# Performance work log

Measured on AMD Instinct MI355X. Metric: run time of the kernel, lower is better.

## Reference

```python
import jax, jax.numpy as jnp
import numpy as np

NUM_HEADS = 8
NUM_KV_HEADS = 1
HEAD_DIM = 256
ROPE_THETA = 10000.0


def setup_inputs() -> dict:
    key = jax.random.key(0)
    ks = jax.random.split(key, 5)
    B, S, H = 4, 2048, 2048
    hidden_states = jax.random.normal(ks[0], (B, S, H), dtype=jnp.float32)
    # Linear weights stored as (in_features, out_features); y = x @ W
    scale = 0.02
    Wq = jax.random.normal(ks[1], (H, NUM_HEADS * HEAD_DIM), dtype=jnp.float32) * scale
    Wk = jax.random.normal(ks[2], (H, NUM_KV_HEADS * HEAD_DIM), dtype=jnp.float32) * scale
    Wv = jax.random.normal(ks[3], (H, NUM_KV_HEADS * HEAD_DIM), dtype=jnp.float32) * scale
    Wo = jax.random.normal(ks[4], (NUM_HEADS * HEAD_DIM, H), dtype=jnp.float32) * scale
    position_ids = jnp.broadcast_to(jnp.arange(S, dtype=jnp.int64), (B, S))
    return {"hidden_states": hidden_states, "Wq": Wq, "Wk": Wk, "Wv": Wv,
            "Wo": Wo, "position_ids": position_ids}


def _rotate_half(x):
    h = x.shape[-1] // 2
    return jnp.concatenate([-x[..., h:], x[..., :h]], axis=-1)


def _rope_cos_sin(position_ids, head_dim, theta):
    # inv_freq: [head_dim/2]
    inv_freq = 1.0 / (theta ** (jnp.arange(0, head_dim, 2, dtype=jnp.float32) / head_dim))
    freqs = position_ids.astype(jnp.float32)[..., None] * inv_freq  # [B,S,hd/2]
    emb = jnp.concatenate([freqs, freqs], axis=-1)                   # [B,S,hd]
    # shape [B,1,S,hd] to broadcast over heads
    return jnp.cos(emb)[:, None], jnp.sin(emb)[:, None]


def reference(hidden_states, Wq, Wk, Wv, Wo, position_ids):
    B, S, H = hidden_states.shape
    groups = NUM_HEADS // NUM_KV_HEADS

    q = (hidden_states @ Wq).reshape(B, S, NUM_HEADS, HEAD_DIM).transpose(0, 2, 1, 3)
    k = (hidden_states @ Wk).reshape(B, S, NUM_KV_HEADS, HEAD_DIM).transpose(0, 2, 1, 3)
    v = (hidden_states @ Wv).reshape(B, S, NUM_KV_HEADS, HEAD_DIM).transpose(0, 2, 1, 3)

    cos, sin = _rope_cos_sin(position_ids, HEAD_DIM, ROPE_THETA)
    q = q * cos + _rotate_half(q) * sin
    k = k * cos + _rotate_half(k) * sin

    # GQA: repeat kv heads to match query heads
    k = jnp.repeat(k, groups, axis=1)  # [B,Hq,S,hd]
    v = jnp.repeat(v, groups, axis=1)

    scores = jnp.einsum('bhqd,bhkd->bhqk', q, k) / jnp.sqrt(jnp.float32(HEAD_DIM))
    causal = position_ids[:, None, :, None] >= position_ids[:, None, None, :]  # [B,1,S,S]
    scores = jnp.where(causal, scores, jnp.float32(-1e9))
    attn = jax.nn.softmax(scores, axis=-1)

    out = jnp.einsum('bhqk,bhkd->bhqd', attn, v)             # [B,H,S,hd]
    out = out.transpose(0, 2, 1, 3).reshape(B, S, NUM_HEADS * HEAD_DIM)
    return out @ Wo
```

## Files before the change

kernel.cpp:

```cpp
#include <hip/hip_runtime.h>
#include <hip/hip_bf16.h>

typedef __bf16 bf16;
typedef __bf16 bf16x8 __attribute__((ext_vector_type(8)));
typedef __bf16 bf16x4 __attribute__((ext_vector_type(4)));
typedef float f32x4 __attribute__((ext_vector_type(4)));

#define NB 4
#define SEQ 2048
#define HID 2048
#define NHEAD 8
#define HDIM 256
#define MTOT (NB*SEQ)

#define WAIT_VM8()  asm volatile("s_waitcnt vmcnt(8)" ::: "memory")
#define WAIT_VM0()  asm volatile("s_waitcnt vmcnt(0)" ::: "memory")

__device__ __forceinline__ void gl_lds16(const void* g, void* l) {
  __builtin_amdgcn_global_load_lds(
      (const __attribute__((address_space(1))) void*)g,
      (__attribute__((address_space(3))) void*)l, 16, 0, 0);
}

__global__ __launch_bounds__(256)
void prologue_kernel(const float* __restrict__ hs, bf16* __restrict__ Xb,
                     const float* __restrict__ Wq, bf16* __restrict__ WqT,
                     const float* __restrict__ Wo, bf16* __restrict__ WoT,
                     const float* __restrict__ Wk, bf16* __restrict__ WkT,
                     const float* __restrict__ Wv, bf16* __restrict__ WvT,
                     float2* __restrict__ tab)
{
  __shared__ float tile[32][33];
  const int bid = blockIdx.x;
  const int t = threadIdx.x;

  if (bid < 8192) {
    size_t i = (size_t)(bid * 256 + t) * 8;
    float4 v0 = *(const float4*)(hs + i);
    float4 v1 = *(const float4*)(hs + i + 4);
    bf16x8 o;
    o[0]=(bf16)v0.x; o[1]=(bf16)v0.y; o[2]=(bf16)v0.z; o[3]=(bf16)v0.w;
    o[4]=(bf16)v1.x; o[5]=(bf16)v1.y; o[6]=(bf16)v1.z; o[7]=(bf16)v1.w;
    *(bf16x8*)(Xb + i) = o;
  } else if (bid < 17408) {
    const float* in; bf16* out; int R, C, bx, by;
    if (bid < 16384) {
      int id = bid - 8192;
      int z = id >> 12, r = id & 4095;
      in = z ? Wo : Wq; out = z ? WoT : WqT; R = 2048; C = 2048;
      bx = (r & 63) * 32; by = (r >> 6) * 32;
    } else {
      int id = bid - 16384;
      int z = id >> 9, r = id & 511;
      in = z ? Wv : Wk; out = z ? WvT : WkT; R = 2048; C = 256;
      bx = (r & 7) * 32; by = (r >> 3) * 32;
    }
    int tx = t & 31, ty = t >> 5;
    #pragma unroll
    for (int k = 0; k < 4; k++)
      tile[ty + 8*k][tx] = in[(size_t)(by + ty + 8*k) * C + bx + tx];
    __syncthreads();
    #pragma unroll
    for (int k = 0; k < 4; k++)
      out[(size_t)(bx + ty + 8*k) * R + by + tx] = (bf16)tile[tx][ty + 8*k];
  } else {
    int i = (bid - 17408) * 256 + t;
    int s = i >> 7, p = i & 127;
    float invf = powf(10000.0f, -(float)p * (1.0f / 128.0f));
    float ang = (float)s * invf;
    float sn, cs;
    sincosf(ang, &sn, &cs);
    tab[i] = make_float2(cs, sn);
  }
}

template<int EPI>
__global__ __launch_bounds__(512, 2)
void gemm256_kernel(const bf16* __restrict__ A, const bf16* __restrict__ Bt,
                    void* __restrict__ Cout, int N, int K,
                    const float2* __restrict__ tab,
                    const bf16* __restrict__ Bt2,
                    bf16* __restrict__ Kout, bf16* __restrict__ VTout)
{
  __shared__ bf16 Albs[2][256 * 64];
  __shared__ bf16 Blbs[2][256 * 64];
  const int t = threadIdx.x, lane = t & 63, w = t >> 6;
  const int g = lane >> 4, c = lane & 15;
  const int wm = w >> 2, wn = w & 3;
  const int bx = blockIdx.x;
  const int m0 = blockIdx.y * 256;

  const bf16* Ab = A + (size_t)m0 * K;
  const bf16* Bb;
  int n0;
  if (EPI == 4 && bx >= 8) { Bb = Bt2 + (size_t)(bx - 8) * 256 * K; n0 = (bx - 8) * 256; }
  else                     { Bb = Bt  + (size_t)bx * 256 * K;       n0 = bx * 256; }

  auto stage = [&](const bf16* G, int k0, bf16* lds) {
    #pragma unroll
    for (int it = 0; it < 4; ++it) {
      int slot = it * 512 + t;
      int row = slot >> 3, part = (slot & 7) ^ (row & 7);
      gl_lds16(G + (size_t)row * K + k0 + part * 8, lds + (it * 512 + w * 64) * 8);
    }
  };

  f32x4 acc[8][4];
  #pragma unroll
  for (int i = 0; i < 8; i++)
    #pragma unroll
    for (int j = 0; j < 4; j++)
      acc[i][j] = (f32x4){0.f, 0.f, 0.f, 0.f};

  stage(Ab, 0, &Albs[0][0]);
  stage(Bb, 0, &Blbs[0][0]);
  __builtin_amdgcn_sched_barrier(0);

  const int NT = K >> 6;
  #pragma unroll 1
  for (int kt = 0; kt < NT; ++kt) {
    const int buf = kt & 1;
    if (kt + 1 < NT) {
      stage(Ab, (kt + 1) * 64, &Albs[buf ^ 1][0]);
      stage(Bb, (kt + 1) * 64, &Blbs[buf ^ 1][0]);
    }
    __builtin_amdgcn_sched_barrier(0);
    if (kt + 1 < NT) { WAIT_VM8(); } else { WAIT_VM0(); }
    __builtin_amdgcn_s_barrier();
    __builtin_amdgcn_sched_barrier(0);

    #pragma unroll
    for (int s2 = 0; s2 < 2; s2++) {
      bf16x8 bfr[4];
      #pragma unroll
      for (int j = 0; j < 4; j++) {
        int row = (EPI == 3 || EPI == 4) ? (wn * 16 + (j & 1) * 64 + (j >> 1) * 128 + c)
                                         : (wn * 64 + j * 16 + c);
        bfr[j] = *(const bf16x8*)((const char*)&Blbs[buf][0] + row * 128 +
                                  ((s2 * 64 + g * 16) ^ ((c & 7) * 16)));
      }
      #pragma unroll
      for (int i = 0; i < 8; i++) {
        int row = wm * 128 + i * 16 + c;
        const bf16x8 af = *(const bf16x8*)((const char*)&Albs[buf][0] + row * 128 +
                                           ((s2 * 64 + g * 16) ^ ((c & 7) * 16)));
        #pragma unroll
        for (int j = 0; j < 4; j++)
          acc[i][j] = __builtin_amdgcn_mfma_f32_16x16x32_bf16(af, bfr[j], acc[i][j], 0, 0, 0);
      }
    }
    __builtin_amdgcn_s_barrier();
  }

  if constexpr (EPI == 4) {
    if (bx < 8) {
      #pragma unroll
      for (int i = 0; i < 8; i++) {
        #pragma unroll
        for (int rr = 0; rr < 4; rr++) {
          int m = m0 + wm * 128 + i * 16 + g * 4 + rr;
          int s = m & (SEQ - 1);
          bf16* orow = (bf16*)Cout + (size_t)m * N + n0;
          #pragma unroll
          for (int jp = 0; jp < 2; jp++) {
            int d = wn * 16 + jp * 64 + c;
            float2 cs = tab[s * 128 + d];
            float vlo = acc[i][jp][rr], vhi = acc[i][jp | 2][rr];
            orow[d]       = (bf16)(vlo * cs.x - vhi * cs.y);
            orow[d + 128] = (bf16)(vhi * cs.x + vlo * cs.y);
          }
        }
      }
    } else if (bx == 8) {
      #pragma unroll
      for (int i = 0; i < 8; i++) {
        #pragma unroll
        for (int rr = 0; rr < 4; rr++) {
          int m = m0 + wm * 128 + i * 16 + g * 4 + rr;
          int s = m & (SEQ - 1);
          bf16* orow = Kout + (size_t)m * 256;
          #pragma unroll
          for (int jp = 0; jp < 2; jp++) {
            int d = wn * 16 + jp * 64 + c;
            float2 cs = tab[s * 128 + d];
            float vlo = acc[i][jp][rr], vhi = acc[i][jp | 2][rr];
            orow[d]       = (bf16)(vlo * cs.x - vhi * cs.y);
            orow[d + 128] = (bf16)(vhi * cs.x + vlo * cs.y);
          }
        }
      }
    } else {
      #pragma unroll
      for (int i = 0; i < 8; i++) {
        #pragma unroll
        for (int rr = 0; rr < 4; rr++) {
          int m = m0 + wm * 128 + i * 16 + g * 4 + rr;
          int b = m >> 11, s = m & 2047;
          #pragma unroll
          for (int j = 0; j < 4; j++) {
            int cl = wn * 16 + (j & 1) * 64 + (j >> 1) * 128 + c;
            VTout[((size_t)b * 256 + cl) * SEQ + s] = (bf16)acc[i][j][rr];
          }
        }
      }
    }
  } else {
    #pragma unroll
    for (int i = 0; i < 8; i++) {
      #pragma unroll
      for (int j = 0; j < 4; j++) {
        #pragma unroll
        for (int rr = 0; rr < 4; rr++) {
          int m = m0 + wm * 128 + i * 16 + g * 4 + rr;
          int col = n0 + wn * 64 + j * 16 + c;
          float v = acc[i][j][rr];
          if constexpr (EPI == 0) ((bf16*)Cout)[(size_t)m * N + col] = (bf16)v;
          else                    ((float*)Cout)[(size_t)m * N + col] = v;
        }
      }
    }
  }
}

__global__ __launch_bounds__(512, 2)
void attn_kernel(const bf16* __restrict__ Q, const bf16* __restrict__ Kb,
                 const bf16* __restrict__ VT, bf16* __restrict__ O)
{
  __shared__ bf16 Klds[2][64 * 256];
  __shared__ bf16 Vlds[2][256 * 64];
  __shared__ bf16 Plds[8][16 * 64];

  const int L = blockIdx.x + ((int)gridDim.x) * blockIdx.y;
  const int xcd = L & 7, slot = L >> 3;
  const int b = xcd >> 1;
  const int rem = ((xcd & 1) << 5) | slot;
  const int h = rem >> 3;
  const int p = rem & 7;

  const int t = threadIdx.x, lane = t & 63, w = t >> 6;
  const int g = lane >> 4, c = lane & 15;

  const bf16* Kbase = Kb + (size_t)b * SEQ * HDIM;
  const bf16* Vbase = VT + (size_t)b * HDIM * SEQ;

  bf16x8 ones8;
  #pragma unroll
  for (int z = 0; z < 8; z++) ones8[z] = (bf16)1.0f;

  auto stageK = [&](int kt, int buf) {
    const int kv0 = kt * 64;
    #pragma unroll
    for (int it = 0; it < 4; ++it) {
      int slot2 = it * 512 + t;
      int krow = slot2 >> 5, kpart = (slot2 & 31) ^ (krow & 7);
      gl_lds16(Kbase + (size_t)(kv0 + krow) * HDIM + kpart * 8,
               &Klds[buf][0] + (it * 512 + w * 64) * 8);
    }
  };
  auto stageV = [&](int kt, int buf) {
    const int kv0 = kt * 64;
    #pragma unroll
    for (int it = 0; it < 4; ++it) {
      int slot2 = it * 512 + t;
      int vrow = slot2 >> 3, vpart = (slot2 & 7) ^ (vrow & 7);
      gl_lds16(Vbase + (size_t)vrow * SEQ + kv0 + vpart * 8,
               &Vlds[buf][0] + (it * 512 + w * 64) * 8);
    }
  };

  #pragma unroll 1
  for (int pass = 0; pass < 2; ++pass) {
    const int qt = pass ? (15 - p) : p;
    const int q0 = qt * 128;
    const int last = 2 * qt + 1;

    bf16x8 qf[8];
    const bf16* qp = Q + (size_t)(b * SEQ + q0 + w * 16 + c) * (NHEAD * HDIM) + h * HDIM + g * 8;
    #pragma unroll
    for (int s = 0; s < 8; s++) qf[s] = *(const bf16x8*)(qp + s * 32);
    __builtin_amdgcn_sched_barrier(0);

    stageK(0, 0);
    stageV(0, 0);
    __builtin_amdgcn_sched_barrier(0);

    f32x4 acc[16];
    #pragma unroll
    for (int f = 0; f < 16; f++) acc[f] = (f32x4){0.f, 0.f, 0.f, 0.f};
    f32x4 acc_s = (f32x4){0.f, 0.f, 0.f, 0.f};

    #pragma unroll 1
    for (int kt = 0; kt <= last; ++kt) {
      const int kv0 = kt * 64;
      const int buf = kt & 1;

      if (kt < last) { stageK(kt + 1, buf ^ 1); stageV(kt + 1, buf ^ 1); }
      __builtin_amdgcn_sched_barrier(0);
      if (kt < last) { WAIT_VM8(); } else { WAIT_VM0(); }
      __builtin_amdgcn_s_barrier();
      __builtin_amdgcn_sched_barrier(0);

      const int qrow_min = q0 + w * 16;
      if (kv0 <= qrow_min + 15) {
        f32x4 sc[4];
        #pragma unroll
        for (int j = 0; j < 4; j++) sc[j] = (f32x4){0.f, 0.f, 0.f, 0.f};
        __builtin_amdgcn_s_setprio(1);
        #pragma unroll
        for (int s = 0; s < 8; s++) {
          #pragma unroll
          for (int j = 0; j < 4; j++) {
            const bf16x8 kf = *(const bf16x8*)((const char*)&Klds[buf][0] + (j * 16 + c) * 512 +
                                               ((s * 64 + g * 16) ^ ((c & 7) * 16)));
            sc[j] = __builtin_amdgcn_mfma_f32_16x16x32_bf16(qf[s], kf, sc[j], 0, 0, 0);
          }
        }
        __builtin_amdgcn_s_setprio(0);

        const float C1 = 0.09016844f;
        const float C2 = 11.54156036f;
        const bool diag = (kv0 + 63 > qrow_min);
        #pragma unroll
        for (int rr = 0; rr < 4; rr++) {
          const int row = g * 4 + rr;
          const int qrow = qrow_min + row;
          #pragma unroll
          for (int j = 0; j < 4; j++) {
            float e = exp2f(__builtin_fmaf(sc[j][rr], C1, -C2));
            if (diag && (kv0 + j * 16 + c > qrow)) e = 0.f;
            *(bf16*)((char*)&Plds[w][0] + row * 128 + (((j * 32) + c * 2) ^ ((row & 7) << 4))) = (bf16)e;
          }
        }

        #pragma unroll
        for (int s2 = 0; s2 < 2; s2++) {
          const bf16x8 pf = *(const bf16x8*)((const char*)&Plds[w][0] + c * 128 +
                                             (((s2 * 4 + g) << 4) ^ ((c & 7) << 4)));
          __builtin_amdgcn_s_setprio(1);
          #pragma unroll
          for (int f = 0; f < 16; f++) {
            const bf16x8 vf = *(const bf16x8*)((const char*)&Vlds[buf][0] + (f * 16 + c) * 128 +
                                               ((s2 * 64 + g * 16) ^ ((c & 7) * 16)));
            acc[f] = __builtin_amdgcn_mfma_f32_16x16x32_bf16(pf, vf, acc[f], 0, 0, 0);
          }
          acc_s = __builtin_amdgcn_mfma_f32_16x16x32_bf16(pf, ones8, acc_s, 0, 0, 0);
          __builtin_amdgcn_s_setprio(0);
        }
      }

      __builtin_amdgcn_s_barrier();
    }

    #pragma unroll
    for (int rr = 0; rr < 4; rr++) {
      float inv = 1.0f / acc_s[rr];
      #pragma unroll
      for (int f = 0; f < 16; f++) {
        float v = acc[f][rr] * inv;
        O[(size_t)(b * SEQ + q0 + w * 16 + g * 4 + rr) * (NHEAD * HDIM) + h * HDIM + f * 16 + c] = (bf16)v;
      }
    }
  }
}

extern "C" void kernel_launch(void* const* d_in, const int* in_sizes, int n_in,
                              void* d_out, int out_size, void* d_ws, size_t ws_size,
                              hipStream_t stream) {
  const float* hs = (const float*)d_in[0];
  const float* Wq = (const float*)d_in[1];
  const float* Wk = (const float*)d_in[2];
  const float* Wv = (const float*)d_in[3];
  const float* Wo = (const float*)d_in[4];

  char* ws = (char*)d_ws;
  bf16* Xb   = (bf16*)(ws + 0);
  bf16* WqT  = (bf16*)(ws + 33554432);
  bf16* WkT  = (bf16*)(ws + 41943040);
  bf16* WvT  = (bf16*)(ws + 42991616);
  bf16* WoT  = (bf16*)(ws + 44040192);
  bf16* Qb   = (bf16*)(ws + 52428800);
  bf16* Kb   = (bf16*)(ws + 85983232);
  bf16* VTb  = (bf16*)(ws + 90177536);
  float2* tab = (float2*)(ws + 94371840);

  prologue_kernel<<<18432, 256, 0, stream>>>(hs, Xb, Wq, WqT, Wo, WoT,
                                             Wk, WkT, Wv, WvT, tab);

  gemm256_kernel<4><<<dim3(10, 32), 512, 0, stream>>>(Xb, WqT, (void*)Qb, 2048, 2048,
                                                      tab, WkT, Kb, VTb);

  attn_kernel<<<dim3(8, 32), 512, 0, stream>>>(Qb, Kb, VTb, Xb );

  gemm256_kernel<2><<<dim3(8, 32), 512, 0, stream>>>(Xb, WoT, d_out, 2048, 2048,
                                                     nullptr, nullptr, nullptr, nullptr);
}
```

Before: 354.9 us.

## Fold K/V projection into Q GEMM blocks as a second small-tile pass

The QKV projection grid shrinks from 10x32 to 8x32 blocks. After its Q tile, each block runs a second GEMM pass over a 64-row by 256-column slice of the K or V projection, with its own RoPE or transposed-V epilogue. The goal is to remove the 64 extra K/V blocks, which overflowed one wave of 256 blocks and formed a tail wave. In exchange every block does a second, less efficient small-tile loop with a shorter A stage and a vmcnt(5) wait.

```diff
diff --git a/kernel.cpp b/kernel.cpp
--- a/kernel.cpp
+++ b/kernel.cpp
@@ -14,6 +14,7 @@
 #define MTOT (NB*SEQ)
 
 #define WAIT_VM8()  asm volatile("s_waitcnt vmcnt(8)" ::: "memory")
+#define WAIT_VM5()  asm volatile("s_waitcnt vmcnt(5)" ::: "memory")
 #define WAIT_VM0()  asm volatile("s_waitcnt vmcnt(0)" ::: "memory")
 
 __device__ __forceinline__ void gl_lds16(const void* g, void* l) {
@@ -88,13 +89,10 @@
   const int g = lane >> 4, c = lane & 15;
   const int wm = w >> 2, wn = w & 3;
   const int bx = blockIdx.x;
-  const int m0 = blockIdx.y * 256;
+  const int m0 = blockIdx.y * 256, n0 = bx * 256;
 
   const bf16* Ab = A + (size_t)m0 * K;
-  const bf16* Bb;
-  int n0;
-  if (EPI == 4 && bx >= 8) { Bb = Bt2 + (size_t)(bx - 8) * 256 * K; n0 = (bx - 8) * 256; }
-  else                     { Bb = Bt  + (size_t)bx * 256 * K;       n0 = bx * 256; }
+  const bf16* Bb = Bt + (size_t)n0 * K;
 
   auto stage = [&](const bf16* G, int k0, bf16* lds) {
     #pragma unroll
@@ -134,8 +132,8 @@
       bf16x8 bfr[4];
       #pragma unroll
       for (int j = 0; j < 4; j++) {
-        int row = (EPI == 3 || EPI == 4) ? (wn * 16 + (j & 1) * 64 + (j >> 1) * 128 + c)
-                                         : (wn * 64 + j * 16 + c);
+        int row = (EPI == 4) ? (wn * 16 + (j & 1) * 64 + (j >> 1) * 128 + c)
+                             : (wn * 64 + j * 16 + c);
         bfr[j] = *(const bf16x8*)((const char*)&Blbs[buf][0] + row * 128 +
                                   ((s2 * 64 + g * 16) ^ ((c & 7) * 16)));
       }
@@ -153,53 +151,113 @@
   }
 
   if constexpr (EPI == 4) {
-    if (bx < 8) {
-      #pragma unroll
-      for (int i = 0; i < 8; i++) {
+    #pragma unroll
+    for (int i = 0; i < 8; i++) {
+      #pragma unroll
+      for (int rr = 0; rr < 4; rr++) {
+        int m = m0 + wm * 128 + i * 16 + g * 4 + rr;
+        int s = m & (SEQ - 1);
+        bf16* orow = (bf16*)Cout + (size_t)m * N + n0;
+        #pragma unroll
+        for (int jp = 0; jp < 2; jp++) {
+          int d = wn * 16 + jp * 64 + c;
+          float2 cs = tab[s * 128 + d];
+          float vlo = acc[i][jp][rr], vhi = acc[i][jp | 2][rr];
+          orow[d]       = (bf16)(vlo * cs.x - vhi * cs.y);
+          orow[d + 128] = (bf16)(vhi * cs.x + vlo * cs.y);
+        }
+      }
+    }
+
+    WAIT_VM0();
+    __builtin_amdgcn_s_barrier();
+    __builtin_amdgcn_sched_barrier(0);
+
+    const int L2 = bx + 8 * blockIdx.y;
+    const int kvm0 = (L2 >> 1) * 64;
+    const int kvc = L2 & 1;
+    const bf16* A2 = A + (size_t)kvm0 * K;
+    const bf16* B2 = Bt2 + (size_t)(kvc * 256) * K;
+
+    auto stageA2 = [&](int k0, bf16* lds) {
+      int row = t >> 3, part = (t & 7) ^ (row & 7);
+      gl_lds16(A2 + (size_t)row * K + k0 + part * 8, lds + (w * 64) * 8);
+    };
+
+    f32x4 acc2[2][4];
+    #pragma unroll
+    for (int i = 0; i < 2; i++)
+      #pragma unroll
+      for (int j = 0; j < 4; j++)
+        acc2[i][j] = (f32x4){0.f, 0.f, 0.f, 0.f};
+
+    stageA2(0, &Albs[0][0]);
+    stage(B2, 0, &Blbs[0][0]);
+    __builtin_amdgcn_sched_barrier(0);
+
+    #pragma unroll 1
+    for (int kt = 0; kt < NT; ++kt) {
+      const int buf = kt & 1;
+      if (kt + 1 < NT) {
+        stageA2((kt + 1) * 64, &Albs[buf ^ 1][0]);
+        stage(B2, (kt + 1) * 64, &Blbs[buf ^ 1][0]);
+      }
+      __builtin_amdgcn_sched_barrier(0);
+      if (kt + 1 < NT) { WAIT_VM5(); } else { WAIT_VM0(); }
+      __builtin_amdgcn_s_barrier();
+      __builtin_amdgcn_sched_barrier(0);
+
+      #pragma unroll
+      for (int s2 = 0; s2 < 2; s2++) {
+        bf16x8 bfr[4];
+        #pragma unroll
+        for (int j = 0; j < 4; j++) {
+          int row = wn * 16 + (j & 1) * 64 + (j >> 1) * 128 + c;
+          bfr[j] = *(const bf16x8*)((const char*)&Blbs[buf][0] + row * 128 +
+                                    ((s2 * 64 + g * 16) ^ ((c & 7) * 16)));
+        }
+        #pragma unroll
+        for (int i = 0; i < 2; i++) {
+          int row = wm * 32 + i * 16 + c;
+          const bf16x8 af = *(const bf16x8*)((const char*)&Albs[buf][0] + row * 128 +
+                                             ((s2 * 64 + g * 16) ^ ((c & 7) * 16)));
+          #pragma unroll
+          for (int j = 0; j < 4; j++)
+            acc2[i][j] = __builtin_amdgcn_mfma_f32_16x16x32_bf16(af, bfr[j], acc2[i][j], 0, 0, 0);
+        }
+      }
+      __builtin_amdgcn_s_barrier();
+    }
+
+    if (kvc == 0) {
+      #pragma unroll
+      for (int i = 0; i < 2; i++) {
         #pragma unroll
         for (int rr = 0; rr < 4; rr++) {
-          int m = m0 + wm * 128 + i * 16 + g * 4 + rr;
+          int m = kvm0 + wm * 32 + i * 16 + g * 4 + rr;
           int s = m & (SEQ - 1);
-          bf16* orow = (bf16*)Cout + (size_t)m * N + n0;
+          bf16* orow = Kout + (size_t)m * 256;
           #pragma unroll
           for (int jp = 0; jp < 2; jp++) {
             int d = wn * 16 + jp * 64 + c;
             float2 cs = tab[s * 128 + d];
-            float vlo = acc[i][jp][rr], vhi = acc[i][jp | 2][rr];
+            float vlo = acc2[i][jp][rr], vhi = acc2[i][jp | 2][rr];
             orow[d]       = (bf16)(vlo * cs.x - vhi * cs.y);
             orow[d + 128] = (bf16)(vhi * cs.x + vlo * cs.y);
           }
         }
       }
-    } else if (bx == 8) {
-      #pragma unroll
-      for (int i = 0; i < 8; i++) {
+    } else {
+      #pragma unroll
+      for (int i = 0; i < 2; i++) {
         #pragma unroll
         for (int rr = 0; rr < 4; rr++) {
-          int m = m0 + wm * 128 + i * 16 + g * 4 + rr;
-          int s = m & (SEQ - 1);
-          bf16* orow = Kout + (size_t)m * 256;
-          #pragma unroll
-          for (int jp = 0; jp < 2; jp++) {
-            int d = wn * 16 + jp * 64 + c;
-            float2 cs = tab[s * 128 + d];
-            float vlo = acc[i][jp][rr], vhi = acc[i][jp | 2][rr];
-            orow[d]       = (bf16)(vlo * cs.x - vhi * cs.y);
-            orow[d + 128] = (bf16)(vhi * cs.x + vlo * cs.y);
-          }
-        }
-      }
-    } else {
-      #pragma unroll
-      for (int i = 0; i < 8; i++) {
-        #pragma unroll
-        for (int rr = 0; rr < 4; rr++) {
-          int m = m0 + wm * 128 + i * 16 + g * 4 + rr;
+          int m = kvm0 + wm * 32 + i * 16 + g * 4 + rr;
           int b = m >> 11, s = m & 2047;
           #pragma unroll
           for (int j = 0; j < 4; j++) {
             int cl = wn * 16 + (j & 1) * 64 + (j >> 1) * 128 + c;
-            VTout[((size_t)b * 256 + cl) * SEQ + s] = (bf16)acc[i][j][rr];
+            VTout[((size_t)b * 256 + cl) * SEQ + s] = (bf16)acc2[i][j][rr];
           }
         }
       }
@@ -386,8 +444,8 @@
   prologue_kernel<<<18432, 256, 0, stream>>>(hs, Xb, Wq, WqT, Wo, WoT,
                                              Wk, WkT, Wv, WvT, tab);
 
-  gemm256_kernel<4><<<dim3(10, 32), 512, 0, stream>>>(Xb, WqT, (void*)Qb, 2048, 2048,
-                                                      tab, WkT, Kb, VTb);
+  gemm256_kernel<4><<<dim3(8, 32), 512, 0, stream>>>(Xb, WqT, (void*)Qb, 2048, 2048,
+                                                     tab, WkT, Kb, VTb);
 
   attn_kernel<<<dim3(8, 32), 512, 0, stream>>>(Qb, Kb, VTb, Xb );
 
```

Result: faster. 309.6 us (-12.8%).
